# Kernel optimization log

Measured on AMD Instinct MI355X. Metric: run time of the kernel, lower is better.

The kernel has to match this reference:

```python
import jax, jax.numpy as jnp
import numpy as np

NB = 4096      # num_batch
NUM = 128      # trajectory samples (P rows)
NVAR = 16      # polynomial coeffs (P cols)
NOBS = 10      # obstacles
NL, NU = 4, 8  # num_lower, num_upper
NPART = NU - NL
T_FIN = 10.0
A_OBS, B_OBS = 6.0, 3.2
RHO_INEQ = RHO_OBS = RHO_LANE = 1.0
V_MIN, V_MAX, A_MAX = 0.1, 30.0, 18.0
MAXITER = 30
W_SM = 100.0


def setup_inputs() -> dict:
    key = jax.random.key(0)
    ks = jax.random.split(key, 13)
    f = jnp.float32
    return {
        'P': jax.random.normal(ks[0], (NUM, NVAR), f),
        'Pdot': jax.random.normal(ks[1], (NUM, NVAR), f),
        'Pddot': jax.random.normal(ks[2], (NUM, NVAR), f),
        'init_state_ego': jax.random.normal(ks[3], (NB, 4), f),
        'fin_state_ego': jax.random.normal(ks[4], (NB, 3), f),
        'closest_obs': jax.random.normal(ks[5], (NB, 2 * NOBS), f),
        'v_obs': jax.random.normal(ks[6], (NB, 2 * NOBS), f),
        'y_ub': jax.random.uniform(ks[7], (NB,), f),
        'y_lb': jax.random.normal(ks[8], (NB,), f),
        'lamda_x': jax.random.normal(ks[9], (NB, NVAR), f),
        'lamda_y': jax.random.normal(ks[10], (NB, NVAR), f),
        'c_x_partial': jax.random.normal(ks[11], (NB, NPART), f),
        'c_y_partial': jax.random.normal(ks[12], (NB, NPART), f),
    }


def _forward(P, Pdot, Pddot, init_state_ego, fin_state_ego, closest_obs, v_obs,
             y_ub, y_lb, lamda_x, lamda_y, c_x_partial, c_y_partial):
    num, nvar = P.shape
    tot_time = jnp.linspace(0.0, T_FIN, num)
    eye = jnp.eye(nvar, dtype=P.dtype)
    A_part = eye[NL:NU]
    A_eq_x = jnp.vstack([P[0], Pdot[0], Pddot[0], Pdot[-1], A_part])            # [4+NPART, nvar]
    A_eq_y = jnp.vstack([P[0], Pdot[0], Pddot[0], P[-1], Pdot[-1], A_part])     # [5+NPART, nvar]
    cost_sm = W_SM * (Pddot.T @ Pddot + 0.1 * eye)
    A_vel, A_acc = Pdot, Pddot
    A_obs_mat = jnp.tile(P, (NOBS, 1))            # [NOBS*num, nvar]
    A_lane = jnp.vstack([P, -P])                  # [2*num, nvar]

    def kkt_inv(cost, A_eq):
        m = A_eq.shape[0]
        top = jnp.hstack([cost, A_eq.T])
        bot = jnp.hstack([A_eq, jnp.zeros((m, m), cost.dtype)])
        return jnp.linalg.inv(jnp.vstack([top, bot]))

    # --- obstacle trajectories: [B, NOBS*num] ---
    x_obs = closest_obs[:, :NOBS]; y_obs = closest_obs[:, NOBS:2 * NOBS]
    vx_obs = v_obs[:, :NOBS];      vy_obs = v_obs[:, NOBS:2 * NOBS]
    x_obs_traj = (x_obs[:, :, None] + vx_obs[:, :, None] * tot_time).reshape(NB, NOBS * num)
    y_obs_traj = (y_obs[:, :, None] + vy_obs[:, :, None] * tot_time).reshape(NB, NOBS * num)

    # --- boundary vectors ---
    x_init = init_state_ego[:, 0:1]; y_init = init_state_ego[:, 1:2]
    v_init = init_state_ego[:, 2:3]; psi_init = init_state_ego[:, 3:4]
    vx_init = v_init * jnp.cos(psi_init); vy_init = v_init * jnp.sin(psi_init)
    zc = jnp.zeros((NB, 1), P.dtype)
    x_fin = fin_state_ego[:, 0:1]; y_fin = fin_state_ego[:, 1:2]
    vx_fin = jnp.clip(fin_state_ego[:, 2:3], V_MIN, V_MAX)  # computed as in original (unused in b_eq)
    b_eq_x = jnp.hstack([x_init, vx_init, zc, x_fin, c_x_partial])
    b_eq_y = jnp.hstack([y_init, vy_init, zc, y_fin, zc, c_y_partial])

    # --- initialization QP (lincost = 0) ---
    cmi_x0 = kkt_inv(cost_sm, A_eq_x)
    cmi_y0 = kkt_inv(cost_sm, A_eq_y)
    sol_x0 = jnp.hstack([jnp.zeros((NB, nvar), P.dtype), b_eq_x]) @ cmi_x0.T
    sol_y0 = jnp.hstack([jnp.zeros((NB, nvar), P.dtype), b_eq_y]) @ cmi_y0.T
    primal_sol = jnp.hstack([sol_x0[:, :nvar], sol_y0[:, :nvar]])

    # --- optimizer KKT inverses ---
    cost_x = cost_sm + RHO_INEQ * (A_acc.T @ A_acc) + RHO_INEQ * (A_vel.T @ A_vel) + RHO_OBS * (A_obs_mat.T @ A_obs_mat)
    cost_y = cost_x + RHO_LANE * (A_lane.T @ A_lane)
    cmi_x = kkt_inv(cost_x, A_eq_x)
    cmi_y = kkt_inv(cost_y, A_eq_y)

    ones_num = jnp.ones((NB, num), P.dtype)
    b_lane = jnp.hstack([y_ub[:, None] * ones_num, -y_lb[:, None] * ones_num])  # [B, 2*num]

    def step(carry, _):
        primal, lx, ly = carry
        cx, cy = primal[:, :nvar], primal[:, nvar:]
        x, xdot, xddot = cx @ P.T, cx @ Pdot.T, cx @ Pddot.T      # [B, num]
        y, ydot, yddot = cy @ P.T, cy @ Pdot.T, cy @ Pddot.T

        wc = jnp.tile(x, (1, NOBS)) - x_obs_traj                   # [B, NOBS*num]
        ws = jnp.tile(y, (1, NOBS)) - y_obs_traj
        alpha_obs = jnp.arctan2(ws * A_OBS, wc * B_OBS)
        co, so = jnp.cos(alpha_obs), jnp.sin(alpha_obs)
        c1 = RHO_OBS * (A_OBS ** 2 * co ** 2 + B_OBS ** 2 * so ** 2)
        c2 = RHO_OBS * (A_OBS * wc * co + B_OBS * ws * so)
        d_obs = jnp.maximum(1.0, c2 / c1)

        alpha_v = jnp.arctan2(ydot, xdot)
        cv, sv = jnp.cos(alpha_v), jnp.sin(alpha_v)
        d_v = jnp.clip(RHO_INEQ * (xdot * cv + ydot * sv) / (RHO_INEQ * (cv ** 2 + sv ** 2)), V_MIN, V_MAX)

        alpha_a = jnp.arctan2(yddot, xddot)
        ca, sa = jnp.cos(alpha_a), jnp.sin(alpha_a)
        d_a = jnp.clip(RHO_INEQ * (xddot * ca + yddot * sa) / (RHO_INEQ * (ca ** 2 + sa ** 2)), 0.0, A_MAX)

        Ay = cy @ A_lane.T                                         # [B, 2*num]
        s_lane = jnp.maximum(0.0, -Ay + b_lane)
        res_lane = Ay - b_lane + s_lane
        res_ax, res_ay = xddot - d_a * ca, yddot - d_a * sa
        res_vx, res_vy = xdot - d_v * cv, ydot - d_v * sv
        res_xo, res_yo = wc - A_OBS * d_obs * co, ws - B_OBS * d_obs * so

        lx = lx - RHO_INEQ * (res_ax @ A_acc) - RHO_INEQ * (res_vx @ A_vel) - RHO_OBS * (res_xo @ A_obs_mat)
        ly = ly - RHO_INEQ * (res_ay @ A_acc) - RHO_INEQ * (res_vy @ A_vel) \
                - RHO_OBS * (res_yo @ A_obs_mat) - RHO_LANE * (res_lane @ A_lane)

        tmp_xo = x_obs_traj + A_OBS * d_obs * co
        tmp_yo = y_obs_traj + B_OBS * d_obs * so
        lincost_x = -lx - RHO_OBS * (tmp_xo @ A_obs_mat) - RHO_INEQ * ((d_a * ca) @ A_acc) - RHO_INEQ * ((d_v * cv) @ A_vel)
        lincost_y = -ly - RHO_OBS * (tmp_yo @ A_obs_mat) - RHO_INEQ * ((d_a * sa) @ A_acc) - RHO_INEQ * ((d_v * sv) @ A_vel) \
                    - RHO_LANE * ((b_lane - s_lane) @ A_lane)
        sol_x = jnp.hstack([-lincost_x, b_eq_x]) @ cmi_x.T
        sol_y = jnp.hstack([-lincost_y, b_eq_y]) @ cmi_y.T
        primal = jnp.hstack([sol_x[:, :nvar], sol_y[:, :nvar]])
        return (primal, lx, ly), None

    (primal_sol, lamda_x, lamda_y), _ = jax.lax.scan(step, (primal_sol, lamda_x, lamda_y), None, length=MAXITER)
    return primal_sol


def reference(P, Pdot, Pddot, init_state_ego, fin_state_ego, closest_obs, v_obs,
              y_ub, y_lb, lamda_x, lamda_y, c_x_partial, c_y_partial):
    return _forward(P, Pdot, Pddot, init_state_ego, fin_state_ego, closest_obs, v_obs,
                    y_ub, y_lb, lamda_x, lamda_y, c_x_partial, c_y_partial)
```

## Files before the change

kernel.cpp:

```cpp
#include <hip/hip_runtime.h>
#include <math.h>

#define NBATCH 4096
#define TNUM   128
#define NOBSC  10
#define MAXIT  30

#define WS_MX   0
#define WS_MY   256
#define WS_MGX  512
#define WS_MGY  768
#define WS_NX   1024
#define WS_NY   1152
#define WS_NX0  1296
#define WS_NY0  1424

#define RS 36

typedef float f32x2 __attribute__((ext_vector_type(2)));
union F4 { float4 v; float f[4]; };
union F2 { float2 v; float f[2]; };

__device__ __forceinline__ f32x2 pfma(f32x2 a, f32x2 b, f32x2 c) {
  return __builtin_elementwise_fma(a, b, c);
}

__device__ __forceinline__ float qsum(float v) {
  float s = v + __int_as_float(__builtin_amdgcn_update_dpp(
      0, __float_as_int(v), 0xB1, 0xF, 0xF, true));
  s = s + __int_as_float(__builtin_amdgcn_update_dpp(
      0, __float_as_int(s), 0x4E, 0xF, 0xF, true));
  return s;
}

__global__ __launch_bounds__(64) void planner_setup(
    const float* __restrict__ P, const float* __restrict__ Pd, const float* __restrict__ Pdd,
    float* __restrict__ ws)
{
  const int mid = blockIdx.x;
  const int tid = threadIdx.x;
  __shared__ float Af[3][TNUM*16];
  __shared__ double C[16][16];
  __shared__ double G[16][16];
  __shared__ double Ae[9][16];
  __shared__ double aug[25][50];
  __shared__ double fcol[32];
  __shared__ int pivs;

  const bool isY = (mid & 1);
  const int  m   = isY ? 9 : 8;
  const int  n   = 16 + m;
  const int  w   = 2 * n;

  #pragma unroll
  for (int u = 0; u < 2; ++u) {
    const int t = tid + 64*u;
    #pragma unroll
    for (int q = 0; q < 4; ++q) {
      *reinterpret_cast<float4*>(&Af[0][t*16+4*q]) = *reinterpret_cast<const float4*>(P   + t*16 + 4*q);
      *reinterpret_cast<float4*>(&Af[1][t*16+4*q]) = *reinterpret_cast<const float4*>(Pd  + t*16 + 4*q);
      *reinterpret_cast<float4*>(&Af[2][t*16+4*q]) = *reinterpret_cast<const float4*>(Pdd + t*16 + 4*q);
    }
  }
  __syncthreads();

  {
    const int j0 = (tid >> 3) * 2;
    const int k0 = (tid & 7) * 2;
    double acc[3][2][2];
    #pragma unroll
    for (int mm = 0; mm < 3; ++mm)
      #pragma unroll
      for (int a2 = 0; a2 < 2; ++a2)
        #pragma unroll
        for (int b2 = 0; b2 < 2; ++b2) acc[mm][a2][b2] = 0.0;
    for (int t = 0; t < TNUM; ++t) {
      #pragma unroll
      for (int mm = 0; mm < 3; ++mm) {
        F2 aj, ak;
        aj.v = *reinterpret_cast<const float2*>(&Af[mm][t*16 + j0]);
        ak.v = *reinterpret_cast<const float2*>(&Af[mm][t*16 + k0]);
        #pragma unroll
        for (int a2 = 0; a2 < 2; ++a2)
          #pragma unroll
          for (int b2 = 0; b2 < 2; ++b2)
            acc[mm][a2][b2] += (double)aj.f[a2] * (double)ak.f[b2];
      }
    }
    const double wsc = isY ? 12.0 : 10.0;
    #pragma unroll
    for (int a2 = 0; a2 < 2; ++a2) {
      #pragma unroll
      for (int b2 = 0; b2 < 2; ++b2) {
        const int j = j0 + a2, kk = k0 + b2;
        const double gdd = acc[2][a2][b2], gd = acc[1][a2][b2], g0 = acc[0][a2][b2];
        const double cs = 100.0 * (gdd + ((j == kk) ? 0.1 : 0.0));
        const double g  = gdd + gd + wsc * g0;
        G[j][kk] = g;
        C[j][kk] = (mid >= 2) ? (cs + g) : cs;
      }
    }
  }
  if (tid < 16) {
    const int j = tid;
    Ae[0][j] = (double)P  [0*16+j];
    Ae[1][j] = (double)Pd [0*16+j];
    Ae[2][j] = (double)Pdd[0*16+j];
    if (!isY) {
      Ae[3][j] = (double)Pd[127*16+j];
      for (int r = 4; r < 8; ++r) Ae[r][j] = (j == r) ? 1.0 : 0.0;
    } else {
      Ae[3][j] = (double)P [127*16+j];
      Ae[4][j] = (double)Pd[127*16+j];
      for (int r = 5; r < 9; ++r) Ae[r][j] = (j == (r-1)) ? 1.0 : 0.0;
    }
  }
  __syncthreads();

  for (int e = tid; e < n * w; e += 64) {
    const int r = e / w, c = e % w;
    double val;
    if (c < n) {
      if (r < 16) val = (c < 16) ? C[r][c] : Ae[c-16][r];
      else        val = (c < 16) ? Ae[r-16][c] : 0.0;
    } else {
      val = ((c - n) == r) ? 1.0 : 0.0;
    }
    aug[r][c] = val;
  }
  __syncthreads();

  const int hw  = (w + 1) >> 1;
  const int rw  = tid >> 1;
  const int hf  = tid & 1;
  for (int kk = 0; kk < n; ++kk) {
    {
      double a = (tid >= kk && tid < n) ? fabs(aug[tid][kk]) : -1.0;
      int p = tid;
      #pragma unroll
      for (int off = 1; off < 64; off <<= 1) {
        const double oa = __shfl_xor(a, off);
        const int    op = __shfl_xor(p, off);
        if (oa > a || (oa == a && op < p)) { a = oa; p = op; }
      }
      if (tid == 0) pivs = p;
    }
    __syncthreads();
    const int p = pivs;
    if (p != kk) {
      for (int c = tid; c < w; c += 64) { double t = aug[kk][c]; aug[kk][c] = aug[p][c]; aug[p][c] = t; }
    }
    __syncthreads();
    const double ipiv = 1.0 / aug[kk][kk];
    for (int c = tid; c < w; c += 64) aug[kk][c] *= ipiv;
    if (tid < n) fcol[tid] = aug[tid][kk];
    __syncthreads();
    if (rw < n && rw != kk) {
      const double f = fcol[rw];
      const int c0 = hf * hw;
      const int c1 = (c0 + hw < w) ? (c0 + hw) : w;
      for (int c = c0; c < c1; ++c) aug[rw][c] -= f * aug[kk][c];
    }
    __syncthreads();
  }

  if (mid == 0) {
    for (int e = tid; e < 16*8; e += 64) ws[WS_NX0 + e] = (float)aug[e >> 3][n + 16 + (e & 7)];
  } else if (mid == 1) {
    for (int e = tid; e < 16*9; e += 64) ws[WS_NY0 + e] = (float)aug[e / 9][n + 16 + (e % 9)];
  } else if (mid == 2) {
    for (int e = tid; e < 256;  e += 64) ws[WS_MX + e] = (float)aug[e >> 4][n + (e & 15)];
    for (int e = tid; e < 16*8; e += 64) ws[WS_NX + e] = (float)aug[e >> 3][n + 16 + (e & 7)];
  } else {
    for (int e = tid; e < 256;  e += 64) ws[WS_MY + e] = (float)aug[e >> 4][n + (e & 15)];
    for (int e = tid; e < 16*9; e += 64) ws[WS_NY + e] = (float)aug[e / 9][n + 16 + (e % 9)];
  }

  if (mid >= 2) {
    for (int e = tid; e < 256; e += 64) {
      const int j = e >> 4, kk = e & 15;
      double s = 0.0;
      for (int mm = 0; mm < 16; ++mm) s += aug[j][n + mm] * G[mm][kk];
      ws[(mid == 2 ? WS_MGX : WS_MGY) + e] = (float)s;
    }
  }
}

__global__ __launch_bounds__(64) void planner_main(
    const float* __restrict__ P, const float* __restrict__ Pd, const float* __restrict__ Pdd,
    const float* __restrict__ init_state, const float* __restrict__ fin_state,
    const float* __restrict__ cobs, const float* __restrict__ vobs,
    const float* __restrict__ yub_g, const float* __restrict__ ylb_g,
    const float* __restrict__ lamx_g, const float* __restrict__ lamy_g,
    const float* __restrict__ cxp_g, const float* __restrict__ cyp_g,
    const float* __restrict__ ws, float* __restrict__ out)
{
  const int b    = blockIdx.x;
  const int tid  = threadIdx.x;
  const int o32  = tid & 31;
  const int cc   = tid >> 5;
  const int rr   = tid & 15;
  const int side = (tid >> 4) & 1;
  const int q4   = tid >> 2;
  const int k    = tid & 3;

  __shared__ alignas(16) float red[16*RS];
  __shared__ alignas(16) float obsL1[5*64*4];
  __shared__ alignas(16) float cL[32];
  __shared__ alignas(16) float hL[32];

  f32x2 Pr2[2][8], Pdr2[2][8], Pddr2[2][8];
  #pragma unroll
  for (int u = 0; u < 2; ++u) {
    const int t = tid + 64*u;
    #pragma unroll
    for (int q = 0; q < 4; ++q) {
      F4 a, bb, ce;
      a.v  = *reinterpret_cast<const float4*>(P   + t*16 + 4*q);
      bb.v = *reinterpret_cast<const float4*>(Pd  + t*16 + 4*q);
      ce.v = *reinterpret_cast<const float4*>(Pdd + t*16 + 4*q);
      Pr2  [u][2*q+0] = f32x2{a.f[0],  a.f[1]};  Pr2  [u][2*q+1] = f32x2{a.f[2],  a.f[3]};
      Pdr2 [u][2*q+0] = f32x2{bb.f[0], bb.f[1]}; Pdr2 [u][2*q+1] = f32x2{bb.f[2], bb.f[3]};
      Pddr2[u][2*q+0] = f32x2{ce.f[0], ce.f[1]}; Pddr2[u][2*q+1] = f32x2{ce.f[2], ce.f[3]};
    }
  }

  f32x2 xot0r[5], yot0r[5];
  {
    const float tt0 = (float)tid        * (10.0f/127.0f);
    const float tt1 = (float)(tid + 64) * (10.0f/127.0f);
    #pragma unroll
    for (int o5 = 0; o5 < 5; ++o5) {
      const int o = 2*o5;
      const float xo0 = cobs[b*20+o],    xo1 = cobs[b*20+o+1];
      const float yo0 = cobs[b*20+10+o], yo1 = cobs[b*20+11+o];
      const float vx0 = vobs[b*20+o],    vx1 = vobs[b*20+o+1];
      const float vy0 = vobs[b*20+10+o], vy1 = vobs[b*20+11+o];
      xot0r[o5] = f32x2{3.2f*fmaf(vx0,tt0,xo0), 3.2f*fmaf(vx1,tt0,xo1)};
      yot0r[o5] = f32x2{6.0f*fmaf(vy0,tt0,yo0), 6.0f*fmaf(vy1,tt0,yo1)};
      *reinterpret_cast<float4*>(&obsL1[o5*256 + tid*4]) =
          float4{3.2f*fmaf(vx0,tt1,xo1*0.f+xo0), 3.2f*fmaf(vx1,tt1,xo1),
                 6.0f*fmaf(vy0,tt1,yo0),         6.0f*fmaf(vy1,tt1,yo1)};
    }
  }
  const float yub = yub_g[b], ylb = ylb_g[b];

  float lam = (o32 < 16) ? lamx_g[b*16 + o32] : lamy_g[b*16 + (o32 - 16)];

  float constv, myc;
  {
    float beq[9];
    const float vi  = init_state[b*4+2];
    const float psi = init_state[b*4+3];
    if (side == 0) {
      beq[0] = init_state[b*4+0];
      beq[1] = vi * cosf(psi);
      beq[2] = 0.f;
      beq[3] = fin_state[b*3+0];
      #pragma unroll
      for (int i2 = 0; i2 < 4; ++i2) beq[4+i2] = cxp_g[b*4+i2];
      beq[8] = 0.f;
    } else {
      beq[0] = init_state[b*4+1];
      beq[1] = vi * sinf(psi);
      beq[2] = 0.f;
      beq[3] = fin_state[b*3+1];
      beq[4] = 0.f;
      #pragma unroll
      for (int i2 = 0; i2 < 4; ++i2) beq[5+i2] = cyp_g[b*4+i2];
    }
    const int nstr = side ? 9 : 8;
    const float* Np  = ws + (side ? WS_NY  : WS_NX ) + rr*nstr;
    const float* N0p = ws + (side ? WS_NY0 : WS_NX0) + rr*nstr;
    float cv = 0.f, c0 = 0.f;
    #pragma unroll
    for (int mm = 0; mm < 9; ++mm) {
      const float bm = beq[mm];
      cv = fmaf(Np[mm],  bm, cv);
      c0 = fmaf(N0p[mm], bm, c0);
    }
    constv = cv;
    myc    = c0;
  }
  if (tid < 32) cL[tid] = myc;

  const float* Mrow  = ws + (side ? WS_MY  : WS_MX ) + rr*16;
  const float* MGrow = ws + (side ? WS_MGY : WS_MGX) + rr*16;
  const bool  kb2 = (k & 2) != 0;
  const int   k1  = k & 1;

  #pragma unroll 1
  for (int it = 0; it < MAXIT; ++it) {
    __builtin_amdgcn_wave_barrier();
    float x0,y0,xd0,yd0,xdd0,ydd0, x1,y1,xd1,yd1,xdd1,ydd1;
    #pragma unroll
    for (int u = 0; u < 2; ++u) {
      f32x2 xv{},yv{},xdv{},ydv{},xddv{},yddv{};
      #pragma unroll
      for (int q = 0; q < 4; ++q) {
        F4 cx4, cy4;
        cx4.v = *reinterpret_cast<const float4*>(&cL[4*q]);
        cy4.v = *reinterpret_cast<const float4*>(&cL[16 + 4*q]);
        const f32x2 c01 = f32x2{cx4.f[0], cx4.f[1]}, c23 = f32x2{cx4.f[2], cx4.f[3]};
        const f32x2 d01 = f32x2{cy4.f[0], cy4.f[1]}, d23 = f32x2{cy4.f[2], cy4.f[3]};
        xv   = pfma(Pr2  [u][2*q], c01, xv);   xv   = pfma(Pr2  [u][2*q+1], c23, xv);
        yv   = pfma(Pr2  [u][2*q], d01, yv);   yv   = pfma(Pr2  [u][2*q+1], d23, yv);
        xdv  = pfma(Pdr2 [u][2*q], c01, xdv);  xdv  = pfma(Pdr2 [u][2*q+1], c23, xdv);
        ydv  = pfma(Pdr2 [u][2*q], d01, ydv);  ydv  = pfma(Pdr2 [u][2*q+1], d23, ydv);
        xddv = pfma(Pddr2[u][2*q], c01, xddv); xddv = pfma(Pddr2[u][2*q+1], c23, xddv);
        yddv = pfma(Pddr2[u][2*q], d01, yddv); yddv = pfma(Pddr2[u][2*q+1], d23, yddv);
      }
      if (u == 0) {
        x0=xv.x+xv.y; y0=yv.x+yv.y; xd0=xdv.x+xdv.y; yd0=ydv.x+ydv.y;
        xdd0=xddv.x+xddv.y; ydd0=yddv.x+yddv.y;
      } else {
        x1=xv.x+xv.y; y1=yv.x+yv.y; xd1=xdv.x+xdv.y; yd1=ydv.x+ydv.y;
        xdd1=xddv.x+xddv.y; ydd1=yddv.x+yddv.y;
      }
    }

    const float ria0 = rsqrtf(fmaxf(fmaf(xdd0,xdd0,ydd0*ydd0), 1e-36f));
    const float ga10 = 1.0f - fminf(1.0f, 18.0f*ria0);
    const float riv0 = rsqrtf(fmaxf(fmaf(xd0,xd0,yd0*yd0), 1e-36f));
    const float gv10 = 1.0f - fminf(fmaxf(1.0f, 0.1f*riv0), 30.0f*riv0);
    const float ria1 = rsqrtf(fmaxf(fmaf(xdd1,xdd1,ydd1*ydd1), 1e-36f));
    const float ga11 = 1.0f - fminf(1.0f, 18.0f*ria1);
    const float riv1 = rsqrtf(fmaxf(fmaf(xd1,xd1,yd1*yd1), 1e-36f));
    const float gv11 = 1.0f - fminf(fmaxf(1.0f, 0.1f*riv1), 30.0f*riv1);

    f32x2 Sx0{}, Sy0{}, Sx1{}, Sy1{};
    {
      const f32x2 xb0 = f32x2{3.2f*x0, 3.2f*x0}, yb0 = f32x2{6.0f*y0, 6.0f*y0};
      const f32x2 xb1 = f32x2{3.2f*x1, 3.2f*x1}, yb1 = f32x2{6.0f*y1, 6.0f*y1};
      #pragma unroll
      for (int o5 = 0; o5 < 5; ++o5) {
        F4 ob1;
        ob1.v = *reinterpret_cast<const float4*>(&obsL1[o5*256 + tid*4]);
        const f32x2 bw0 = xb0 - xot0r[o5];
        const f32x2 aw0 = yb0 - yot0r[o5];
        const f32x2 bw1 = xb1 - f32x2{ob1.f[0], ob1.f[1]};
        const f32x2 aw1 = yb1 - f32x2{ob1.f[2], ob1.f[3]};
        const f32x2 r20 = pfma(bw0,bw0,aw0*aw0);
        const f32x2 r21 = pfma(bw1,bw1,aw1*aw1);
        const f32x2 ee0 = f32x2{
          fmaxf(fmaf(19.2f, rsqrtf(fmaxf(r20.x,1e-36f)), -1.0f), 0.f),
          fmaxf(fmaf(19.2f, rsqrtf(fmaxf(r20.y,1e-36f)), -1.0f), 0.f)};
        const f32x2 ee1 = f32x2{
          fmaxf(fmaf(19.2f, rsqrtf(fmaxf(r21.x,1e-36f)), -1.0f), 0.f),
          fmaxf(fmaf(19.2f, rsqrtf(fmaxf(r21.y,1e-36f)), -1.0f), 0.f)};
        Sx0 = pfma(ee0, bw0, Sx0);  Sy0 = pfma(ee0, aw0, Sy0);
        Sx1 = pfma(ee1, bw1, Sx1);  Sy1 = pfma(ee1, aw1, Sy1);
      }
    }
    const float c0p0 = -(Sx0.x+Sx0.y)*0.3125f;
    const float rln0 = fmaxf(y0-yub,0.f) - fmaxf(ylb-y0,0.f);
    const float c2p0 = rln0 - (Sy0.x+Sy0.y)*(1.0f/6.0f);
    const float c0dd0 = xdd0*ga10, c0d0 = xd0*gv10;
    const float c2dd0 = ydd0*ga10, c2d0 = yd0*gv10;
    const float c0p1 = -(Sx1.x+Sx1.y)*0.3125f;
    const float rln1 = fmaxf(y1-yub,0.f) - fmaxf(ylb-y1,0.f);
    const float c2p1 = rln1 - (Sy1.x+Sy1.y)*(1.0f/6.0f);
    const float c0dd1 = xdd1*ga11, c0d1 = xd1*gv11;
    const float c2dd1 = ydd1*ga11, c2d1 = yd1*gv11;

    float outv[8];
    #pragma unroll
    for (int s2 = 0; s2 < 8; ++s2) outv[s2] = 0.f;
    {
      const f32x2 A00{c0dd0,c0dd0}, D00{c0d0,c0d0}, Q00{c0p0,c0p0};
      const f32x2 A20{c2dd0,c2dd0}, D20{c2d0,c2d0}, Q20{c2p0,c2p0};
      const f32x2 A01{c0dd1,c0dd1}, D01{c0d1,c0d1}, Q01{c0p1,c0p1};
      const f32x2 A21{c2dd1,c2dd1}, D21{c2d1,c2d1}, Q21{c2p1,c2p1};
      #pragma unroll
      for (int j2 = 0; j2 < 8; ++j2) {
        f32x2 vx = pfma(A00, Pddr2[0][j2], pfma(D00, Pdr2[0][j2], Q00*Pr2[0][j2]));
        vx = pfma(A01, Pddr2[1][j2], pfma(D01, Pdr2[1][j2], pfma(Q01, Pr2[1][j2], vx)));
        f32x2 vy = pfma(A20, Pddr2[0][j2], pfma(D20, Pdr2[0][j2], Q20*Pr2[0][j2]));
        vy = pfma(A21, Pddr2[1][j2], pfma(D21, Pdr2[1][j2], pfma(Q21, Pr2[1][j2], vy)));
        const float qx0 = qsum(vx.x), qx1 = qsum(vx.y);
        const float qy0 = qsum(vy.x), qy1 = qsum(vy.y);
        const float s0 = kb2 ? qy0 : qx0;
        const float s1 = kb2 ? qy1 : qx1;
        const bool match = (k1 == (j2 >> 2));
        const int  sb = 2*(j2 & 3);
        outv[sb]   = match ? s0 : outv[sb];
        outv[sb+1] = match ? s1 : outv[sb+1];
      }
    }
    __builtin_amdgcn_wave_barrier();
    {
      float* wr = red + q4*RS + 8*k;
      *reinterpret_cast<float4*>(wr)     = float4{outv[0],outv[1],outv[2],outv[3]};
      *reinterpret_cast<float4*>(wr + 4) = float4{outv[4],outv[5],outv[6],outv[7]};
    }
    __builtin_amdgcn_wave_barrier();

    float h;
    {
      const float* rd = red + (cc*8)*RS + o32;
      float s = 0.f;
      #pragma unroll
      for (int i = 0; i < 8; ++i) s += rd[i*RS];
      s += __shfl_xor(s, 32);
      lam -= s;
      h = lam - s;
    }
    __builtin_amdgcn_wave_barrier();
    if (tid < 32) hL[tid] = h;
    __builtin_amdgcn_wave_barrier();

    {
      f32x2 accv{};
      #pragma unroll
      for (int q = 0; q < 4; ++q) {
        F4 m4, g4, h4, c4;
        m4.v = *reinterpret_cast<const float4*>(Mrow  + 4*q);
        g4.v = *reinterpret_cast<const float4*>(MGrow + 4*q);
        h4.v = *reinterpret_cast<const float4*>(&hL[side*16 + 4*q]);
        c4.v = *reinterpret_cast<const float4*>(&cL[side*16 + 4*q]);
        accv = pfma(f32x2{m4.f[0],m4.f[1]}, f32x2{h4.f[0],h4.f[1]}, accv);
        accv = pfma(f32x2{g4.f[0],g4.f[1]}, f32x2{c4.f[0],c4.f[1]}, accv);
        accv = pfma(f32x2{m4.f[2],m4.f[3]}, f32x2{h4.f[2],h4.f[3]}, accv);
        accv = pfma(f32x2{g4.f[2],g4.f[3]}, f32x2{c4.f[2],c4.f[3]}, accv);
      }
      myc = constv + accv.x + accv.y;
    }
    __builtin_amdgcn_wave_barrier();
    if (tid < 32) cL[tid] = myc;
  }

  if (tid < 32) out[b*32 + tid] = myc;
}

extern "C" void kernel_launch(void* const* d_in, const int* in_sizes, int n_in,
                              void* d_out, int out_size, void* d_ws, size_t ws_size,
                              hipStream_t stream) {
  const float* P    = (const float*)d_in[0];
  const float* Pd   = (const float*)d_in[1];
  const float* Pdd  = (const float*)d_in[2];
  const float* init = (const float*)d_in[3];
  const float* fin  = (const float*)d_in[4];
  const float* cobs = (const float*)d_in[5];
  const float* vobs = (const float*)d_in[6];
  const float* yub  = (const float*)d_in[7];
  const float* ylb  = (const float*)d_in[8];
  const float* lamx = (const float*)d_in[9];
  const float* lamy = (const float*)d_in[10];
  const float* cxp  = (const float*)d_in[11];
  const float* cyp  = (const float*)d_in[12];
  float* ws  = (float*)d_ws;
  float* o   = (float*)d_out;

  planner_setup<<<dim3(4), dim3(64), 0, stream>>>(P, Pd, Pdd, ws);
  planner_main<<<dim3(NBATCH), dim3(64), 0, stream>>>(
      P, Pd, Pdd, init, fin, cobs, vobs, yub, ylb, lamx, lamy, cxp, cyp, ws, o);
}
```

Before: 209.2 us.

## Process two batch elements per wavefront to raise instruction-level parallelism

```diff
diff --git a/kernel.cpp b/kernel.cpp
--- a/kernel.cpp
+++ b/kernel.cpp
@@ -195,8 +195,9 @@
     const float* __restrict__ cxp_g, const float* __restrict__ cyp_g,
     const float* __restrict__ ws, float* __restrict__ out)
 {
-  const int b    = blockIdx.x;
   const int tid  = threadIdx.x;
+  const int b0   = blockIdx.x * 2;
+  const int b1   = b0 + 1;
   const int o32  = tid & 31;
   const int cc   = tid >> 5;
   const int rr   = tid & 15;
@@ -204,10 +205,10 @@
   const int q4   = tid >> 2;
   const int k    = tid & 3;
 
-  __shared__ alignas(16) float red[16*RS];
-  __shared__ alignas(16) float obsL1[5*64*4];
-  __shared__ alignas(16) float cL[32];
-  __shared__ alignas(16) float hL[32];
+  __shared__ alignas(16) float red[2][16*RS];
+  __shared__ alignas(16) float obsL1[2][5*64*4];
+  __shared__ alignas(16) float cL[2][32];
+  __shared__ alignas(16) float hL[2][32];
 
   f32x2 Pr2[2][8], Pdr2[2][8], Pddr2[2][8];
   #pragma unroll
@@ -225,64 +226,85 @@
     }
   }
 
-  f32x2 xot0r[5], yot0r[5];
+  f32x2 xot0A[5], yot0A[5], xot0B[5], yot0B[5];
   {
     const float tt0 = (float)tid        * (10.0f/127.0f);
     const float tt1 = (float)(tid + 64) * (10.0f/127.0f);
     #pragma unroll
     for (int o5 = 0; o5 < 5; ++o5) {
       const int o = 2*o5;
-      const float xo0 = cobs[b*20+o],    xo1 = cobs[b*20+o+1];
-      const float yo0 = cobs[b*20+10+o], yo1 = cobs[b*20+11+o];
-      const float vx0 = vobs[b*20+o],    vx1 = vobs[b*20+o+1];
-      const float vy0 = vobs[b*20+10+o], vy1 = vobs[b*20+11+o];
-      xot0r[o5] = f32x2{3.2f*fmaf(vx0,tt0,xo0), 3.2f*fmaf(vx1,tt0,xo1)};
-      yot0r[o5] = f32x2{6.0f*fmaf(vy0,tt0,yo0), 6.0f*fmaf(vy1,tt0,yo1)};
-      *reinterpret_cast<float4*>(&obsL1[o5*256 + tid*4]) =
-          float4{3.2f*fmaf(vx0,tt1,xo1*0.f+xo0), 3.2f*fmaf(vx1,tt1,xo1),
-                 6.0f*fmaf(vy0,tt1,yo0),         6.0f*fmaf(vy1,tt1,yo1)};
-    }
-  }
-  const float yub = yub_g[b], ylb = ylb_g[b];
-
-  float lam = (o32 < 16) ? lamx_g[b*16 + o32] : lamy_g[b*16 + (o32 - 16)];
-
-  float constv, myc;
+      {
+        const float xo0 = cobs[b0*20+o],    xo1 = cobs[b0*20+o+1];
+        const float yo0 = cobs[b0*20+10+o], yo1 = cobs[b0*20+11+o];
+        const float vx0 = vobs[b0*20+o],    vx1 = vobs[b0*20+o+1];
+        const float vy0 = vobs[b0*20+10+o], vy1 = vobs[b0*20+11+o];
+        xot0A[o5] = f32x2{3.2f*fmaf(vx0,tt0,xo0), 3.2f*fmaf(vx1,tt0,xo1)};
+        yot0A[o5] = f32x2{6.0f*fmaf(vy0,tt0,yo0), 6.0f*fmaf(vy1,tt0,yo1)};
+        *reinterpret_cast<float4*>(&obsL1[0][o5*256 + tid*4]) =
+            float4{3.2f*fmaf(vx0,tt1,xo0), 3.2f*fmaf(vx1,tt1,xo1),
+                   6.0f*fmaf(vy0,tt1,yo0), 6.0f*fmaf(vy1,tt1,yo1)};
+      }
+      {
+        const float xo0 = cobs[b1*20+o],    xo1 = cobs[b1*20+o+1];
+        const float yo0 = cobs[b1*20+10+o], yo1 = cobs[b1*20+11+o];
+        const float vx0 = vobs[b1*20+o],    vx1 = vobs[b1*20+o+1];
+        const float vy0 = vobs[b1*20+10+o], vy1 = vobs[b1*20+11+o];
+        xot0B[o5] = f32x2{3.2f*fmaf(vx0,tt0,xo0), 3.2f*fmaf(vx1,tt0,xo1)};
+        yot0B[o5] = f32x2{6.0f*fmaf(vy0,tt0,yo0), 6.0f*fmaf(vy1,tt0,yo1)};
+        *reinterpret_cast<float4*>(&obsL1[1][o5*256 + tid*4]) =
+            float4{3.2f*fmaf(vx0,tt1,xo0), 3.2f*fmaf(vx1,tt1,xo1),
+                   6.0f*fmaf(vy0,tt1,yo0), 6.0f*fmaf(vy1,tt1,yo1)};
+      }
+    }
+  }
+  const float yubA = yub_g[b0], ylbA = ylb_g[b0];
+  const float yubB = yub_g[b1], ylbB = ylb_g[b1];
+
+  float lamA = (o32 < 16) ? lamx_g[b0*16 + o32] : lamy_g[b0*16 + (o32 - 16)];
+  float lamB = (o32 < 16) ? lamx_g[b1*16 + o32] : lamy_g[b1*16 + (o32 - 16)];
+
+  float constvA, mycA, constvB, mycB;
   {
-    float beq[9];
-    const float vi  = init_state[b*4+2];
-    const float psi = init_state[b*4+3];
-    if (side == 0) {
-      beq[0] = init_state[b*4+0];
-      beq[1] = vi * cosf(psi);
-      beq[2] = 0.f;
-      beq[3] = fin_state[b*3+0];
-      #pragma unroll
-      for (int i2 = 0; i2 < 4; ++i2) beq[4+i2] = cxp_g[b*4+i2];
-      beq[8] = 0.f;
-    } else {
-      beq[0] = init_state[b*4+1];
-      beq[1] = vi * sinf(psi);
-      beq[2] = 0.f;
-      beq[3] = fin_state[b*3+1];
-      beq[4] = 0.f;
-      #pragma unroll
-      for (int i2 = 0; i2 < 4; ++i2) beq[5+i2] = cyp_g[b*4+i2];
-    }
     const int nstr = side ? 9 : 8;
     const float* Np  = ws + (side ? WS_NY  : WS_NX ) + rr*nstr;
     const float* N0p = ws + (side ? WS_NY0 : WS_NX0) + rr*nstr;
-    float cv = 0.f, c0 = 0.f;
-    #pragma unroll
-    for (int mm = 0; mm < 9; ++mm) {
-      const float bm = beq[mm];
-      cv = fmaf(Np[mm],  bm, cv);
-      c0 = fmaf(N0p[mm], bm, c0);
-    }
-    constv = cv;
-    myc    = c0;
-  }
-  if (tid < 32) cL[tid] = myc;
+    float nrow[9], n0row[9];
+    #pragma unroll
+    for (int mm = 0; mm < 9; ++mm) { nrow[mm] = Np[mm]; n0row[mm] = N0p[mm]; }
+
+    float beq[9];
+    #pragma unroll
+    for (int pb = 0; pb < 2; ++pb) {
+      const int b = pb ? b1 : b0;
+      const float vi  = init_state[b*4+2];
+      const float psi = init_state[b*4+3];
+      if (side == 0) {
+        beq[0] = init_state[b*4+0];
+        beq[1] = vi * cosf(psi);
+        beq[2] = 0.f;
+        beq[3] = fin_state[b*3+0];
+        #pragma unroll
+        for (int i2 = 0; i2 < 4; ++i2) beq[4+i2] = cxp_g[b*4+i2];
+        beq[8] = 0.f;
+      } else {
+        beq[0] = init_state[b*4+1];
+        beq[1] = vi * sinf(psi);
+        beq[2] = 0.f;
+        beq[3] = fin_state[b*3+1];
+        beq[4] = 0.f;
+        #pragma unroll
+        for (int i2 = 0; i2 < 4; ++i2) beq[5+i2] = cyp_g[b*4+i2];
+      }
+      float cv = 0.f, c0 = 0.f;
+      #pragma unroll
+      for (int mm = 0; mm < 9; ++mm) {
+        cv = fmaf(nrow[mm],  beq[mm], cv);
+        c0 = fmaf(n0row[mm], beq[mm], c0);
+      }
+      if (pb == 0) { constvA = cv; mycA = c0; if (tid < 32) cL[0][tid] = c0; }
+      else         { constvB = cv; mycB = c0; if (tid < 32) cL[1][tid] = c0; }
+    }
+  }
 
   const float* Mrow  = ws + (side ? WS_MY  : WS_MX ) + rr*16;
   const float* MGrow = ws + (side ? WS_MGY : WS_MGX) + rr*16;
@@ -292,144 +314,178 @@
   #pragma unroll 1
   for (int it = 0; it < MAXIT; ++it) {
     __builtin_amdgcn_wave_barrier();
-    float x0,y0,xd0,yd0,xdd0,ydd0, x1,y1,xd1,yd1,xdd1,ydd1;
-    #pragma unroll
-    for (int u = 0; u < 2; ++u) {
-      f32x2 xv{},yv{},xdv{},ydv{},xddv{},yddv{};
+    float x0A,y0A,xd0A,yd0A,xdd0A,ydd0A, x1A,y1A,xd1A,yd1A,xdd1A,ydd1A;
+    float x0B,y0B,xd0B,yd0B,xdd0B,ydd0B, x1B,y1B,xd1B,yd1B,xdd1B,ydd1B;
+    #pragma unroll
+    for (int pb = 0; pb < 2; ++pb) {
+      const float* cW = cL[pb];
+      #pragma unroll
+      for (int u = 0; u < 2; ++u) {
+        f32x2 xv{},yv{},xdv{},ydv{},xddv{},yddv{};
+        #pragma unroll
+        for (int q = 0; q < 4; ++q) {
+          F4 cx4, cy4;
+          cx4.v = *reinterpret_cast<const float4*>(&cW[4*q]);
+          cy4.v = *reinterpret_cast<const float4*>(&cW[16 + 4*q]);
+          const f32x2 c01 = f32x2{cx4.f[0], cx4.f[1]}, c23 = f32x2{cx4.f[2], cx4.f[3]};
+          const f32x2 d01 = f32x2{cy4.f[0], cy4.f[1]}, d23 = f32x2{cy4.f[2], cy4.f[3]};
+          xv   = pfma(Pr2  [u][2*q], c01, xv);   xv   = pfma(Pr2  [u][2*q+1], c23, xv);
+          yv   = pfma(Pr2  [u][2*q], d01, yv);   yv   = pfma(Pr2  [u][2*q+1], d23, yv);
+          xdv  = pfma(Pdr2 [u][2*q], c01, xdv);  xdv  = pfma(Pdr2 [u][2*q+1], c23, xdv);
+          ydv  = pfma(Pdr2 [u][2*q], d01, ydv);  ydv  = pfma(Pdr2 [u][2*q+1], d23, ydv);
+          xddv = pfma(Pddr2[u][2*q], c01, xddv); xddv = pfma(Pddr2[u][2*q+1], c23, xddv);
+          yddv = pfma(Pddr2[u][2*q], d01, yddv); yddv = pfma(Pddr2[u][2*q+1], d23, yddv);
+        }
+        const float xs = xv.x+xv.y,   ys = yv.x+yv.y;
+        const float xds = xdv.x+xdv.y, yds = ydv.x+ydv.y;
+        const float xdds = xddv.x+xddv.y, ydds = yddv.x+yddv.y;
+        if (pb == 0) {
+          if (u == 0) { x0A=xs; y0A=ys; xd0A=xds; yd0A=yds; xdd0A=xdds; ydd0A=ydds; }
+          else        { x1A=xs; y1A=ys; xd1A=xds; yd1A=yds; xdd1A=xdds; ydd1A=ydds; }
+        } else {
+          if (u == 0) { x0B=xs; y0B=ys; xd0B=xds; yd0B=yds; xdd0B=xdds; ydd0B=ydds; }
+          else        { x1B=xs; y1B=ys; xd1B=xds; yd1B=yds; xdd1B=xdds; ydd1B=ydds; }
+        }
+      }
+    }
+
+    #pragma unroll
+    for (int pb = 0; pb < 2; ++pb) {
+      const float x0   = pb ? x0B   : x0A,   y0   = pb ? y0B   : y0A;
+      const float xd0  = pb ? xd0B  : xd0A,  yd0  = pb ? yd0B  : yd0A;
+      const float xdd0 = pb ? xdd0B : xdd0A, ydd0 = pb ? ydd0B : ydd0A;
+      const float x1   = pb ? x1B   : x1A,   y1   = pb ? y1B   : y1A;
+      const float xd1  = pb ? xd1B  : xd1A,  yd1  = pb ? yd1B  : yd1A;
+      const float xdd1 = pb ? xdd1B : xdd1A, ydd1 = pb ? ydd1B : ydd1A;
+      const float yub  = pb ? yubB : yubA,   ylb  = pb ? ylbB : ylbA;
+      const f32x2* xot0r = pb ? xot0B : xot0A;
+      const f32x2* yot0r = pb ? yot0B : yot0A;
+      const float* obsW  = obsL1[pb];
+
+      const float ria0 = rsqrtf(fmaxf(fmaf(xdd0,xdd0,ydd0*ydd0), 1e-36f));
+      const float ga10 = 1.0f - fminf(1.0f, 18.0f*ria0);
+      const float riv0 = rsqrtf(fmaxf(fmaf(xd0,xd0,yd0*yd0), 1e-36f));
+      const float gv10 = 1.0f - fminf(fmaxf(1.0f, 0.1f*riv0), 30.0f*riv0);
+      const float ria1 = rsqrtf(fmaxf(fmaf(xdd1,xdd1,ydd1*ydd1), 1e-36f));
+      const float ga11 = 1.0f - fminf(1.0f, 18.0f*ria1);
+      const float riv1 = rsqrtf(fmaxf(fmaf(xd1,xd1,yd1*yd1), 1e-36f));
+      const float gv11 = 1.0f - fminf(fmaxf(1.0f, 0.1f*riv1), 30.0f*riv1);
+
+      f32x2 Sx0{}, Sy0{}, Sx1{}, Sy1{};
+      {
+        const f32x2 xb0 = f32x2{3.2f*x0, 3.2f*x0}, yb0 = f32x2{6.0f*y0, 6.0f*y0};
+        const f32x2 xb1 = f32x2{3.2f*x1, 3.2f*x1}, yb1 = f32x2{6.0f*y1, 6.0f*y1};
+        #pragma unroll
+        for (int o5 = 0; o5 < 5; ++o5) {
+          F4 ob1;
+          ob1.v = *reinterpret_cast<const float4*>(&obsW[o5*256 + tid*4]);
+          const f32x2 bw0 = xb0 - xot0r[o5];
+          const f32x2 aw0 = yb0 - yot0r[o5];
+          const f32x2 bw1 = xb1 - f32x2{ob1.f[0], ob1.f[1]};
+          const f32x2 aw1 = yb1 - f32x2{ob1.f[2], ob1.f[3]};
+          const f32x2 r20 = pfma(bw0,bw0,aw0*aw0);
+          const f32x2 r21 = pfma(bw1,bw1,aw1*aw1);
+          const f32x2 ee0 = f32x2{
+            fmaxf(fmaf(19.2f, rsqrtf(fmaxf(r20.x,1e-36f)), -1.0f), 0.f),
+            fmaxf(fmaf(19.2f, rsqrtf(fmaxf(r20.y,1e-36f)), -1.0f), 0.f)};
+          const f32x2 ee1 = f32x2{
+            fmaxf(fmaf(19.2f, rsqrtf(fmaxf(r21.x,1e-36f)), -1.0f), 0.f),
+            fmaxf(fmaf(19.2f, rsqrtf(fmaxf(r21.y,1e-36f)), -1.0f), 0.f)};
+          Sx0 = pfma(ee0, bw0, Sx0);  Sy0 = pfma(ee0, aw0, Sy0);
+          Sx1 = pfma(ee1, bw1, Sx1);  Sy1 = pfma(ee1, aw1, Sy1);
+        }
+      }
+      const float c0p0 = -(Sx0.x+Sx0.y)*0.3125f;
+      const float rln0 = fmaxf(y0-yub,0.f) - fmaxf(ylb-y0,0.f);
+      const float c2p0 = rln0 - (Sy0.x+Sy0.y)*(1.0f/6.0f);
+      const float c0dd0 = xdd0*ga10, c0d0 = xd0*gv10;
+      const float c2dd0 = ydd0*ga10, c2d0 = yd0*gv10;
+      const float c0p1 = -(Sx1.x+Sx1.y)*0.3125f;
+      const float rln1 = fmaxf(y1-yub,0.f) - fmaxf(ylb-y1,0.f);
+      const float c2p1 = rln1 - (Sy1.x+Sy1.y)*(1.0f/6.0f);
+      const float c0dd1 = xdd1*ga11, c0d1 = xd1*gv11;
+      const float c2dd1 = ydd1*ga11, c2d1 = yd1*gv11;
+
+      float outv[8];
+      #pragma unroll
+      for (int s2 = 0; s2 < 8; ++s2) outv[s2] = 0.f;
+      {
+        const f32x2 A00{c0dd0,c0dd0}, D00{c0d0,c0d0}, Q00{c0p0,c0p0};
+        const f32x2 A20{c2dd0,c2dd0}, D20{c2d0,c2d0}, Q20{c2p0,c2p0};
+        const f32x2 A01{c0dd1,c0dd1}, D01{c0d1,c0d1}, Q01{c0p1,c0p1};
+        const f32x2 A21{c2dd1,c2dd1}, D21{c2d1,c2d1}, Q21{c2p1,c2p1};
+        #pragma unroll
+        for (int j2 = 0; j2 < 8; ++j2) {
+          f32x2 vx = pfma(A00, Pddr2[0][j2], pfma(D00, Pdr2[0][j2], Q00*Pr2[0][j2]));
+          vx = pfma(A01, Pddr2[1][j2], pfma(D01, Pdr2[1][j2], pfma(Q01, Pr2[1][j2], vx)));
+          f32x2 vy = pfma(A20, Pddr2[0][j2], pfma(D20, Pdr2[0][j2], Q20*Pr2[0][j2]));
+          vy = pfma(A21, Pddr2[1][j2], pfma(D21, Pdr2[1][j2], pfma(Q21, Pr2[1][j2], vy)));
+          const float qx0 = qsum(vx.x), qx1 = qsum(vx.y);
+          const float qy0 = qsum(vy.x), qy1 = qsum(vy.y);
+          const float s0 = kb2 ? qy0 : qx0;
+          const float s1 = kb2 ? qy1 : qx1;
+          const bool match = (k1 == (j2 >> 2));
+          const int  sb = 2*(j2 & 3);
+          outv[sb]   = match ? s0 : outv[sb];
+          outv[sb+1] = match ? s1 : outv[sb+1];
+        }
+      }
+      __builtin_amdgcn_wave_barrier();
+      {
+        float* wr = red[pb] + q4*RS + 8*k;
+        *reinterpret_cast<float4*>(wr)     = float4{outv[0],outv[1],outv[2],outv[3]};
+        *reinterpret_cast<float4*>(wr + 4) = float4{outv[4],outv[5],outv[6],outv[7]};
+      }
+    }
+    __builtin_amdgcn_wave_barrier();
+
+    {
+      const float* rdA = red[0] + (cc*8)*RS + o32;
+      const float* rdB = red[1] + (cc*8)*RS + o32;
+      float sA = 0.f, sB = 0.f;
+      #pragma unroll
+      for (int i = 0; i < 8; ++i) { sA += rdA[i*RS]; sB += rdB[i*RS]; }
+      sA += __shfl_xor(sA, 32);
+      sB += __shfl_xor(sB, 32);
+      lamA -= sA;
+      lamB -= sB;
+      const float hA = lamA - sA;
+      const float hB = lamB - sB;
+      __builtin_amdgcn_wave_barrier();
+      if (tid < 32) { hL[0][tid] = hA; hL[1][tid] = hB; }
+      __builtin_amdgcn_wave_barrier();
+    }
+
+    {
+      f32x2 accA{}, accB{};
       #pragma unroll
       for (int q = 0; q < 4; ++q) {
-        F4 cx4, cy4;
-        cx4.v = *reinterpret_cast<const float4*>(&cL[4*q]);
-        cy4.v = *reinterpret_cast<const float4*>(&cL[16 + 4*q]);
-        const f32x2 c01 = f32x2{cx4.f[0], cx4.f[1]}, c23 = f32x2{cx4.f[2], cx4.f[3]};
-        const f32x2 d01 = f32x2{cy4.f[0], cy4.f[1]}, d23 = f32x2{cy4.f[2], cy4.f[3]};
-        xv   = pfma(Pr2  [u][2*q], c01, xv);   xv   = pfma(Pr2  [u][2*q+1], c23, xv);
-        yv   = pfma(Pr2  [u][2*q], d01, yv);   yv   = pfma(Pr2  [u][2*q+1], d23, yv);
-        xdv  = pfma(Pdr2 [u][2*q], c01, xdv);  xdv  = pfma(Pdr2 [u][2*q+1], c23, xdv);
-        ydv  = pfma(Pdr2 [u][2*q], d01, ydv);  ydv  = pfma(Pdr2 [u][2*q+1], d23, ydv);
-        xddv = pfma(Pddr2[u][2*q], c01, xddv); xddv = pfma(Pddr2[u][2*q+1], c23, xddv);
-        yddv = pfma(Pddr2[u][2*q], d01, yddv); yddv = pfma(Pddr2[u][2*q+1], d23, yddv);
-      }
-      if (u == 0) {
-        x0=xv.x+xv.y; y0=yv.x+yv.y; xd0=xdv.x+xdv.y; yd0=ydv.x+ydv.y;
-        xdd0=xddv.x+xddv.y; ydd0=yddv.x+yddv.y;
-      } else {
-        x1=xv.x+xv.y; y1=yv.x+yv.y; xd1=xdv.x+xdv.y; yd1=ydv.x+ydv.y;
-        xdd1=xddv.x+xddv.y; ydd1=yddv.x+yddv.y;
-      }
-    }
-
-    const float ria0 = rsqrtf(fmaxf(fmaf(xdd0,xdd0,ydd0*ydd0), 1e-36f));
-    const float ga10 = 1.0f - fminf(1.0f, 18.0f*ria0);
-    const float riv0 = rsqrtf(fmaxf(fmaf(xd0,xd0,yd0*yd0), 1e-36f));
-    const float gv10 = 1.0f - fminf(fmaxf(1.0f, 0.1f*riv0), 30.0f*riv0);
-    const float ria1 = rsqrtf(fmaxf(fmaf(xdd1,xdd1,ydd1*ydd1), 1e-36f));
-    const float ga11 = 1.0f - fminf(1.0f, 18.0f*ria1);
-    const float riv1 = rsqrtf(fmaxf(fmaf(xd1,xd1,yd1*yd1), 1e-36f));
-    const float gv11 = 1.0f - fminf(fmaxf(1.0f, 0.1f*riv1), 30.0f*riv1);
-
-    f32x2 Sx0{}, Sy0{}, Sx1{}, Sy1{};
-    {
-      const f32x2 xb0 = f32x2{3.2f*x0, 3.2f*x0}, yb0 = f32x2{6.0f*y0, 6.0f*y0};
-      const f32x2 xb1 = f32x2{3.2f*x1, 3.2f*x1}, yb1 = f32x2{6.0f*y1, 6.0f*y1};
-      #pragma unroll
-      for (int o5 = 0; o5 < 5; ++o5) {
-        F4 ob1;
-        ob1.v = *reinterpret_cast<const float4*>(&obsL1[o5*256 + tid*4]);
-        const f32x2 bw0 = xb0 - xot0r[o5];
-        const f32x2 aw0 = yb0 - yot0r[o5];
-        const f32x2 bw1 = xb1 - f32x2{ob1.f[0], ob1.f[1]};
-        const f32x2 aw1 = yb1 - f32x2{ob1.f[2], ob1.f[3]};
-        const f32x2 r20 = pfma(bw0,bw0,aw0*aw0);
-        const f32x2 r21 = pfma(bw1,bw1,aw1*aw1);
-        const f32x2 ee0 = f32x2{
-          fmaxf(fmaf(19.2f, rsqrtf(fmaxf(r20.x,1e-36f)), -1.0f), 0.f),
-          fmaxf(fmaf(19.2f, rsqrtf(fmaxf(r20.y,1e-36f)), -1.0f), 0.f)};
-        const f32x2 ee1 = f32x2{
-          fmaxf(fmaf(19.2f, rsqrtf(fmaxf(r21.x,1e-36f)), -1.0f), 0.f),
-          fmaxf(fmaf(19.2f, rsqrtf(fmaxf(r21.y,1e-36f)), -1.0f), 0.f)};
-        Sx0 = pfma(ee0, bw0, Sx0);  Sy0 = pfma(ee0, aw0, Sy0);
-        Sx1 = pfma(ee1, bw1, Sx1);  Sy1 = pfma(ee1, aw1, Sy1);
-      }
-    }
-    const float c0p0 = -(Sx0.x+Sx0.y)*0.3125f;
-    const float rln0 = fmaxf(y0-yub,0.f) - fmaxf(ylb-y0,0.f);
-    const float c2p0 = rln0 - (Sy0.x+Sy0.y)*(1.0f/6.0f);
-    const float c0dd0 = xdd0*ga10, c0d0 = xd0*gv10;
-    const float c2dd0 = ydd0*ga10, c2d0 = yd0*gv10;
-    const float c0p1 = -(Sx1.x+Sx1.y)*0.3125f;
-    const float rln1 = fmaxf(y1-yub,0.f) - fmaxf(ylb-y1,0.f);
-    const float c2p1 = rln1 - (Sy1.x+Sy1.y)*(1.0f/6.0f);
-    const float c0dd1 = xdd1*ga11, c0d1 = xd1*gv11;
-    const float c2dd1 = ydd1*ga11, c2d1 = yd1*gv11;
-
-    float outv[8];
-    #pragma unroll
-    for (int s2 = 0; s2 < 8; ++s2) outv[s2] = 0.f;
-    {
-      const f32x2 A00{c0dd0,c0dd0}, D00{c0d0,c0d0}, Q00{c0p0,c0p0};
-      const f32x2 A20{c2dd0,c2dd0}, D20{c2d0,c2d0}, Q20{c2p0,c2p0};
-      const f32x2 A01{c0dd1,c0dd1}, D01{c0d1,c0d1}, Q01{c0p1,c0p1};
-      const f32x2 A21{c2dd1,c2dd1}, D21{c2d1,c2d1}, Q21{c2p1,c2p1};
-      #pragma unroll
-      for (int j2 = 0; j2 < 8; ++j2) {
-        f32x2 vx = pfma(A00, Pddr2[0][j2], pfma(D00, Pdr2[0][j2], Q00*Pr2[0][j2]));
-        vx = pfma(A01, Pddr2[1][j2], pfma(D01, Pdr2[1][j2], pfma(Q01, Pr2[1][j2], vx)));
-        f32x2 vy = pfma(A20, Pddr2[0][j2], pfma(D20, Pdr2[0][j2], Q20*Pr2[0][j2]));
-        vy = pfma(A21, Pddr2[1][j2], pfma(D21, Pdr2[1][j2], pfma(Q21, Pr2[1][j2], vy)));
-        const float qx0 = qsum(vx.x), qx1 = qsum(vx.y);
-        const float qy0 = qsum(vy.x), qy1 = qsum(vy.y);
-        const float s0 = kb2 ? qy0 : qx0;
-        const float s1 = kb2 ? qy1 : qx1;
-        const bool match = (k1 == (j2 >> 2));
-        const int  sb = 2*(j2 & 3);
-        outv[sb]   = match ? s0 : outv[sb];
-        outv[sb+1] = match ? s1 : outv[sb+1];
-      }
+        F4 m4, g4, hA4, cA4, hB4, cB4;
+        m4.v  = *reinterpret_cast<const float4*>(Mrow  + 4*q);
+        g4.v  = *reinterpret_cast<const float4*>(MGrow + 4*q);
+        hA4.v = *reinterpret_cast<const float4*>(&hL[0][side*16 + 4*q]);
+        cA4.v = *reinterpret_cast<const float4*>(&cL[0][side*16 + 4*q]);
+        hB4.v = *reinterpret_cast<const float4*>(&hL[1][side*16 + 4*q]);
+        cB4.v = *reinterpret_cast<const float4*>(&cL[1][side*16 + 4*q]);
+        const f32x2 m01 = f32x2{m4.f[0], m4.f[1]}, m23 = f32x2{m4.f[2], m4.f[3]};
+        const f32x2 g01 = f32x2{g4.f[0], g4.f[1]}, g23 = f32x2{g4.f[2], g4.f[3]};
+        accA = pfma(m01, f32x2{hA4.f[0], hA4.f[1]}, accA);
+        accA = pfma(g01, f32x2{cA4.f[0], cA4.f[1]}, accA);
+        accA = pfma(m23, f32x2{hA4.f[2], hA4.f[3]}, accA);
+        accA = pfma(g23, f32x2{cA4.f[2], cA4.f[3]}, accA);
+        accB = pfma(m01, f32x2{hB4.f[0], hB4.f[1]}, accB);
+        accB = pfma(g01, f32x2{cB4.f[0], cB4.f[1]}, accB);
+        accB = pfma(m23, f32x2{hB4.f[2], hB4.f[3]}, accB);
+        accB = pfma(g23, f32x2{cB4.f[2], cB4.f[3]}, accB);
+      }
+      mycA = constvA + accA.x + accA.y;
+      mycB = constvB + accB.x + accB.y;
     }
     __builtin_amdgcn_wave_barrier();
-    {
-      float* wr = red + q4*RS + 8*k;
-      *reinterpret_cast<float4*>(wr)     = float4{outv[0],outv[1],outv[2],outv[3]};
-      *reinterpret_cast<float4*>(wr + 4) = float4{outv[4],outv[5],outv[6],outv[7]};
-    }
-    __builtin_amdgcn_wave_barrier();
-
-    float h;
-    {
-      const float* rd = red + (cc*8)*RS + o32;
-      float s = 0.f;
-      #pragma unroll
-      for (int i = 0; i < 8; ++i) s += rd[i*RS];
-      s += __shfl_xor(s, 32);
-      lam -= s;
-      h = lam - s;
-    }
-    __builtin_amdgcn_wave_barrier();
-    if (tid < 32) hL[tid] = h;
-    __builtin_amdgcn_wave_barrier();
-
-    {
-      f32x2 accv{};
-      #pragma unroll
-      for (int q = 0; q < 4; ++q) {
-        F4 m4, g4, h4, c4;
-        m4.v = *reinterpret_cast<const float4*>(Mrow  + 4*q);
-        g4.v = *reinterpret_cast<const float4*>(MGrow + 4*q);
-        h4.v = *reinterpret_cast<const float4*>(&hL[side*16 + 4*q]);
-        c4.v = *reinterpret_cast<const float4*>(&cL[side*16 + 4*q]);
-        accv = pfma(f32x2{m4.f[0],m4.f[1]}, f32x2{h4.f[0],h4.f[1]}, accv);
-        accv = pfma(f32x2{g4.f[0],g4.f[1]}, f32x2{c4.f[0],c4.f[1]}, accv);
-        accv = pfma(f32x2{m4.f[2],m4.f[3]}, f32x2{h4.f[2],h4.f[3]}, accv);
-        accv = pfma(f32x2{g4.f[2],g4.f[3]}, f32x2{c4.f[2],c4.f[3]}, accv);
-      }
-      myc = constv + accv.x + accv.y;
-    }
-    __builtin_amdgcn_wave_barrier();
-    if (tid < 32) cL[tid] = myc;
-  }
-
-  if (tid < 32) out[b*32 + tid] = myc;
+    if (tid < 32) { cL[0][tid] = mycA; cL[1][tid] = mycB; }
+  }
+
+  if (tid < 32) { out[b0*32 + tid] = mycA; out[b1*32 + tid] = mycB; }
 }
 
 extern "C" void kernel_launch(void* const* d_in, const int* in_sizes, int n_in,
@@ -452,6 +508,6 @@
   float* o   = (float*)d_out;
 
   planner_setup<<<dim3(4), dim3(64), 0, stream>>>(P, Pd, Pdd, ws);
-  planner_main<<<dim3(NBATCH), dim3(64), 0, stream>>>(
+  planner_main<<<dim3(NBATCH/2), dim3(64), 0, stream>>>(
       P, Pd, Pdd, init, fin, cobs, vobs, yub, ylb, lamx, lamy, cxp, cyp, ws, o);
 }
```

Result: slower. 241.7 us (+15.5%).
